# Optimization experiments

Measured on AMD Instinct MI355X. Metric: run time of the kernel, lower is better.

Reference implementation:

```python
import jax, jax.numpy as jnp
import numpy as np

N, V, H, LAT, OUT = 256, 256, 256, 64, 128
EPS = 1e-5

def setup_inputs() -> dict:
    key = jax.random.key(0)
    ks = jax.random.split(key, 16)
    s = lambda fan_in: 1.0 / np.sqrt(fan_in)
    gin = 2 * H + LAT  # GAT input size
    return {
        "obs": jax.random.normal(ks[0], (N, V, 5), jnp.float32),
        "high_intention": jax.random.normal(ks[1], (N, V, LAT), jnp.float32),
        "Ws": jax.random.uniform(ks[2], (2, H), jnp.float32, -s(2), s(2)),
        "bs": jax.random.uniform(ks[3], (H,), jnp.float32, -s(2), s(2)),
        "Wv": jax.random.uniform(ks[4], (2, H), jnp.float32, -s(2), s(2)),
        "bv": jax.random.uniform(ks[5], (H,), jnp.float32, -s(2), s(2)),
        "Wg": jax.random.uniform(ks[6], (gin, H), jnp.float32, -s(gin), s(gin)),
        "a_w": jax.random.uniform(ks[7], (2 * H,), jnp.float32, -s(2 * H), s(2 * H)),
        "W1": jax.random.uniform(ks[8], (2 * H, H), jnp.float32, -s(2 * H), s(2 * H)),
        "b1": jax.random.uniform(ks[9], (H,), jnp.float32, -s(2 * H), s(2 * H)),
        "g1": jnp.ones((H,), jnp.float32),
        "be1": jnp.zeros((H,), jnp.float32),
        "W2": jax.random.uniform(ks[10], (H, OUT), jnp.float32, -s(H), s(H)),
        "b2": jax.random.uniform(ks[11], (OUT,), jnp.float32, -s(H), s(H)),
        "g2": jnp.ones((OUT,), jnp.float32),
        "be2": jnp.zeros((OUT,), jnp.float32),
    }

def _batchnorm(x, g, b):
    # training-mode BatchNorm1d: batch stats, biased variance
    m = x.mean(0)
    v = x.var(0)
    return g * (x - m) / jnp.sqrt(v + EPS) + b

def reference(obs, high_intention, Ws, bs, Wv, bv, Wg, a_w, W1, b1, g1, be1, W2, b2, g2, be2):
    se = jax.nn.relu(obs[:, :, 1:3] @ Ws + bs)   # [N,V,H]
    ve = jax.nn.relu(obs[:, :, 3:5] @ Wv + bv)   # [N,V,H]
    comb = jnp.concatenate([se, ve, high_intention], axis=-1)  # [N,V,2H+LAT]
    h = comb @ Wg                                 # [N,V,H]
    hdim = Ws.shape[1]
    a1, a2 = a_w[:hdim], a_w[hdim:]
    # e_ij = leaky_relu(a . [h_i, h_j]) = leaky_relu(h_i.a1 + h_j.a2)
    e = jax.nn.leaky_relu((h @ a1)[:, :, None] + (h @ a2)[:, None, :], 0.01)  # [N,V,V]
    att = jax.nn.softmax(e, axis=2)
    h_prime = jnp.einsum('nij,njh->nih', att, h)  # [N,V,H]
    cf = jnp.concatenate([h_prime, se], axis=-1).reshape(-1, 2 * hdim)
    x = jax.nn.relu(_batchnorm(cf @ W1 + b1, g1, be1))
    x = jax.nn.relu(_batchnorm(x @ W2 + b2, g2, be2))
    return x.reshape(obs.shape[0], obs.shape[1], -1)
```

## Files before the change

### kernel.cpp

```cpp
#include <hip/hip_runtime.h>
#include <math.h>

namespace {

constexpr int kH = 256, kOut = 128;
constexpr int kNV = 65536;
constexpr float kEps = 1e-5f;

typedef __attribute__((ext_vector_type(8))) short bf16x8;
typedef __attribute__((ext_vector_type(4))) float f32x4;
typedef unsigned int u32;

__device__ inline short f2bf(float f) {
  union { float f; u32 u; } v; v.f = f;
  u32 r = v.u + 0x7fffu + ((v.u >> 16) & 1u);
  return (short)(r >> 16);
}
__device__ inline float bf2f(short s) {
  union { float f; u32 u; } v; v.u = ((u32)(unsigned short)s) << 16; return v.f;
}

__global__ __launch_bounds__(256) void kpack(
    const float* __restrict__ Wg, const float* __restrict__ W1,
    const float* __restrict__ W2, const float* __restrict__ a_w,
    short* __restrict__ wgp, short* __restrict__ w1p, short* __restrict__ w2p,
    short* __restrict__ wgab, float* __restrict__ st)
{
  const int bid = blockIdx.x, t = threadIdx.x;
  if (bid >= 152) {
    const int b = bid - 152;
    if (t < 144) {
      const int col = t & 1, k = b * 72 + (t >> 1);
      if (k < 576) {
        const float* rowp = Wg + (size_t)k * 256;
        const float* ap = a_w + col * 256;
        float s0 = 0.f, s1 = 0.f, s2 = 0.f, s3 = 0.f;
        for (int c = 0; c < 256; c += 4) {
          s0 = fmaf(rowp[c+0], ap[c+0], s0);
          s1 = fmaf(rowp[c+1], ap[c+1], s1);
          s2 = fmaf(rowp[c+2], ap[c+2], s2);
          s3 = fmaf(rowp[c+3], ap[c+3], s3);
        }
        const int ks = k >> 5, r = k & 31, hq = r >> 3, e = r & 7;
        wgab[((ks*2 + col)*4 + hq)*8 + e] = f2bf((s0 + s1) + (s2 + s3));
      }
    }
    return;
  }
  if (bid == 0) {
#pragma unroll
    for (int i = 0; i < 6; ++i) st[i*256 + t] = 0.f;
  }
  const int uid = bid * 256 + t;
  const float* src; short* dst; int N; int u;
  if (uid < 18432)            { src = Wg; dst = wgp; N = 256; u = uid; }
  else if (uid < 34816)       { src = W1; dst = w1p; N = 256; u = uid - 18432; }
  else if (uid < 38912)       { src = W2; dst = w2p; N = 128; u = uid - 34816; }
  else return;
  const int lane = u & 63, ctkt = u >> 6;
  const int nct = N >> 4;
  const int kt = ctkt / nct, ct = ctkt % nct;
  const int row = kt * 32 + (lane >> 4) * 8;
  const int col = ct * 16 + (lane & 15);
  bf16x8 ov;
#pragma unroll
  for (int e = 0; e < 8; ++e) ov[e] = f2bf(src[(size_t)(row + e) * N + col]);
  *reinterpret_cast<bf16x8*>(dst + (size_t)u * 8) = ov;
}

__global__ __launch_bounds__(256, 4) void k1_encode(
    const float* __restrict__ obs, const float* __restrict__ hin,
    const float* __restrict__ Ws, const float* __restrict__ bs,
    const float* __restrict__ Wv, const float* __restrict__ bv,
    const short* __restrict__ wgp, const short* __restrict__ wgab,
    short* __restrict__ hpack, float* __restrict__ ha1, float* __restrict__ ha2)
{
  __shared__ __align__(16) short comb[32][584];
  __shared__ float obs_s[32][4];
  const int t = threadIdx.x;
  const int xcd = blockIdx.x & 7, ib = blockIdx.x >> 3;
  const int workid = xcd * 256 + ib;
  const int r0 = workid * 32;

  if (t < 128) obs_s[t >> 2][t & 3] = obs[(size_t)(r0 + (t >> 2)) * 5 + 1 + (t & 3)];
#pragma unroll
  for (int jj = 0; jj < 2; ++jj) {
    const int f = jj * 1024 + t * 4;
    const int row = f >> 6, c = f & 63;
    const float4 v = *reinterpret_cast<const float4*>(hin + (size_t)r0 * 64 + f);
    short4 o;
    o.x = f2bf(v.x); o.y = f2bf(v.y); o.z = f2bf(v.z); o.w = f2bf(v.w);
    *reinterpret_cast<short4*>(&comb[row][512 + c]) = o;
  }
  const float ws0 = Ws[t], ws1 = Ws[256 + t], bsv = bs[t];
  const float wv0 = Wv[t], wv1 = Wv[256 + t], bvv = bv[t];
  __syncthreads();
  for (int r = 0; r < 32; ++r) {
    const float o1 = obs_s[r][0], o2 = obs_s[r][1], o3 = obs_s[r][2], o4 = obs_s[r][3];
    const float sv = fmaf(o2, ws1, fmaf(o1, ws0, bsv));
    comb[r][t] = f2bf(fmaxf(sv, 0.f));
    const float vv = fmaf(o4, wv1, fmaf(o3, wv0, bvv));
    comb[r][256 + t] = f2bf(fmaxf(vv, 0.f));
  }
  __syncthreads();

  const int w = t >> 6, lane = t & 63, lo = lane & 15, hq = lane >> 4;
  f32x4 acc[2][4];
  f32x4 accE[2];
#pragma unroll
  for (int rt = 0; rt < 2; ++rt) {
    accE[rt] = (f32x4){0.f, 0.f, 0.f, 0.f};
#pragma unroll
    for (int ct = 0; ct < 4; ++ct) acc[rt][ct] = (f32x4){0.f, 0.f, 0.f, 0.f};
  }

  const short* wB = wgp + ((size_t)(w*4)*64 + lane)*8;
  bf16x8 bb[4];
#pragma unroll
  for (int ct = 0; ct < 4; ++ct)
    bb[ct] = *reinterpret_cast<const bf16x8*>(wB + ct*512);

#pragma unroll
  for (int ks = 0; ks < 18; ++ks) {
    bf16x8 bn[4];
    if (ks < 17) {
#pragma unroll
      for (int ct = 0; ct < 4; ++ct)
        bn[ct] = *reinterpret_cast<const bf16x8*>(wB + (ks+1)*8192 + ct*512);
    }
    bf16x8 a[2];
#pragma unroll
    for (int rt = 0; rt < 2; ++rt)
      a[rt] = *reinterpret_cast<const bf16x8*>(&comb[rt*16 + lo][ks*32 + hq*8]);
#pragma unroll
    for (int rt = 0; rt < 2; ++rt)
#pragma unroll
      for (int ct = 0; ct < 4; ++ct)
        acc[rt][ct] = __builtin_amdgcn_mfma_f32_16x16x32_bf16(a[rt], bb[ct], acc[rt][ct], 0, 0, 0);
    if (w == 0) {
      bf16x8 be;
      if (lo < 2)
        be = *reinterpret_cast<const bf16x8*>(wgab + ((ks*2 + lo)*4 + hq)*8);
      else
        be = (bf16x8){0,0,0,0,0,0,0,0};
#pragma unroll
      for (int rt = 0; rt < 2; ++rt)
        accE[rt] = __builtin_amdgcn_mfma_f32_16x16x32_bf16(a[rt], be, accE[rt], 0, 0, 0);
    }
    if (ks < 17) {
#pragma unroll
      for (int ct = 0; ct < 4; ++ct) bb[ct] = bn[ct];
    }
  }
  if (w == 0 && lo < 2) {
    float* dst = (lo == 0) ? ha1 : ha2;
#pragma unroll
    for (int rt = 0; rt < 2; ++rt)
#pragma unroll
      for (int q = 0; q < 4; ++q)
        dst[r0 + rt*16 + hq*4 + q] = accE[rt][q];
  }
  __syncthreads();

  short* pimg = reinterpret_cast<short*>(&comb[0][0]);
#pragma unroll
  for (int rt = 0; rt < 2; ++rt)
#pragma unroll
    for (int ct = 0; ct < 4; ++ct) {
      const int base = (((w*4 + ct)*64) + (rt*2 + (hq>>1))*16 + lo)*8 + (hq&1)*4;
      short4 val;
      val.x = f2bf(acc[rt][ct][0]); val.y = f2bf(acc[rt][ct][1]);
      val.z = f2bf(acc[rt][ct][2]); val.w = f2bf(acc[rt][ct][3]);
      *reinterpret_cast<short4*>(pimg + base) = val;
    }
  __syncthreads();

  short* dst = hpack + (size_t)workid * 8192;
#pragma unroll
  for (int j = 0; j < 4; ++j)
    *reinterpret_cast<bf16x8*>(dst + j*2048 + t*8) =
        *reinterpret_cast<const bf16x8*>(pimg + j*2048 + t*8);
}

__global__ __launch_bounds__(256, 4) void k23_attn_fc1(
    const float* __restrict__ ha1g, const float* __restrict__ ha2g,
    const short* __restrict__ hpack, const float* __restrict__ obs,
    const float* __restrict__ Ws, const float* __restrict__ bs,
    const short* __restrict__ w1p, short* __restrict__ y, float* __restrict__ st)
{
  __shared__ __align__(16) short attimg[64][264];
  __shared__ float ws_s[768];
  __shared__ float ha2_s[256];
  __shared__ float ha1_s[64], rd_s[64];
  __shared__ float red[4][64];
  __shared__ float obs_s[64][2];
  const int t = threadIdx.x;
  const int xcd = blockIdx.x & 7, ib = blockIdx.x >> 3;
  const int workid = xcd * 128 + ib;
  const int r0 = workid * 64;
  const int n = r0 >> 8;

  ws_s[t] = Ws[t]; ws_s[256 + t] = Ws[256 + t]; ws_s[512 + t] = bs[t];
  ha2_s[t] = ha2g[n*256 + t];
  if (t < 64) ha1_s[t] = ha1g[r0 + t];
  if (t < 128) obs_s[t >> 1][t & 1] = obs[(size_t)(r0 + (t >> 1)) * 5 + 1 + (t & 1)];
  __syncthreads();

  const int rr = t & 63, seg = t >> 6;
  {
    const float a1 = ha1_s[rr];
    float sum = 0.f;
    for (int c8 = 0; c8 < 8; ++c8) {
      bf16x8 pk;
#pragma unroll
      for (int e = 0; e < 8; ++e) {
        float x = a1 + ha2_s[seg*64 + c8*8 + e];
        x = fmaxf(x, 0.01f * x);
        const float ev = __expf(x);
        sum += ev;
        pk[e] = f2bf(ev);
      }
      *reinterpret_cast<bf16x8*>(&attimg[rr][seg*64 + c8*8]) = pk;
    }
    red[seg][rr] = sum;
  }
  __syncthreads();
  if (t < 64) rd_s[t] = 1.f / (red[0][t] + red[1][t] + red[2][t] + red[3][t]);
  __syncthreads();

  const int w = t >> 6, lane = t & 63, lo = lane & 15, hq = lane >> 4;
  f32x4 acc[4][4];
#pragma unroll
  for (int rt = 0; rt < 4; ++rt)
#pragma unroll
    for (int ct = 0; ct < 4; ++ct) acc[rt][ct] = (f32x4){0.f, 0.f, 0.f, 0.f};

  {
    const short* bB = hpack + (size_t)n*65536 + ((size_t)(w*4)*64 + lane)*8;
    bf16x8 bb[4];
#pragma unroll
    for (int ct = 0; ct < 4; ++ct) bb[ct] = *reinterpret_cast<const bf16x8*>(bB + ct*512);
    for (int ks = 0; ks < 8; ++ks) {
      bf16x8 bn[4];
      if (ks < 7) {
#pragma unroll
        for (int ct = 0; ct < 4; ++ct)
          bn[ct] = *reinterpret_cast<const bf16x8*>(bB + (ks+1)*8192 + ct*512);
      }
      bf16x8 a[4];
#pragma unroll
      for (int rt = 0; rt < 4; ++rt)
        a[rt] = *reinterpret_cast<const bf16x8*>(&attimg[rt*16 + lo][ks*32 + hq*8]);
#pragma unroll
      for (int rt = 0; rt < 4; ++rt)
#pragma unroll
        for (int ct = 0; ct < 4; ++ct)
          acc[rt][ct] = __builtin_amdgcn_mfma_f32_16x16x32_bf16(a[rt], bb[ct], acc[rt][ct], 0, 0, 0);
      if (ks < 7) {
#pragma unroll
        for (int ct = 0; ct < 4; ++ct) bb[ct] = bn[ct];
      }
    }
  }
  __syncthreads();

#pragma unroll
  for (int rt = 0; rt < 4; ++rt)
#pragma unroll
    for (int q = 0; q < 4; ++q) {
      const int row = rt*16 + hq*4 + q;
      const float sc = rd_s[row];
#pragma unroll
      for (int ct = 0; ct < 4; ++ct)
        attimg[row][w*64 + ct*16 + lo] = f2bf(acc[rt][ct][q] * sc);
    }
  __syncthreads();

  f32x4 accY[4][4];
#pragma unroll
  for (int rt = 0; rt < 4; ++rt)
#pragma unroll
    for (int ct = 0; ct < 4; ++ct) accY[rt][ct] = (f32x4){0.f, 0.f, 0.f, 0.f};
  const short* w1B = w1p + ((size_t)(w*4)*64 + lane)*8;
  {
    bf16x8 bb[4];
#pragma unroll
    for (int ct = 0; ct < 4; ++ct) bb[ct] = *reinterpret_cast<const bf16x8*>(w1B + ct*512);
    for (int ks = 0; ks < 8; ++ks) {
      bf16x8 bn[4];
      if (ks < 7) {
#pragma unroll
        for (int ct = 0; ct < 4; ++ct)
          bn[ct] = *reinterpret_cast<const bf16x8*>(w1B + (ks+1)*8192 + ct*512);
      }
      bf16x8 a[4];
#pragma unroll
      for (int rt = 0; rt < 4; ++rt)
        a[rt] = *reinterpret_cast<const bf16x8*>(&attimg[rt*16 + lo][ks*32 + hq*8]);
#pragma unroll
      for (int rt = 0; rt < 4; ++rt)
#pragma unroll
        for (int ct = 0; ct < 4; ++ct)
          accY[rt][ct] = __builtin_amdgcn_mfma_f32_16x16x32_bf16(a[rt], bb[ct], accY[rt][ct], 0, 0, 0);
      if (ks < 7) {
#pragma unroll
        for (int ct = 0; ct < 4; ++ct) bb[ct] = bn[ct];
      }
    }
  }
  __syncthreads();

  {
    const float o1 = obs_s[rr][0], o2 = obs_s[rr][1];
    for (int c8 = 0; c8 < 8; ++c8) {
      const int c = seg*64 + c8*8;
      bf16x8 pk;
#pragma unroll
      for (int e = 0; e < 8; ++e) {
        const float sv = fmaf(o2, ws_s[256 + c + e], fmaf(o1, ws_s[c + e], ws_s[512 + c + e]));
        pk[e] = f2bf(fmaxf(sv, 0.f));
      }
      *reinterpret_cast<bf16x8*>(&attimg[rr][c]) = pk;
    }
  }
  __syncthreads();

  {
    bf16x8 bb[4];
#pragma unroll
    for (int ct = 0; ct < 4; ++ct)
      bb[ct] = *reinterpret_cast<const bf16x8*>(w1B + 8*8192 + ct*512);
    for (int ks = 0; ks < 8; ++ks) {
      bf16x8 bn[4];
      if (ks < 7) {
#pragma unroll
        for (int ct = 0; ct < 4; ++ct)
          bn[ct] = *reinterpret_cast<const bf16x8*>(w1B + (ks+9)*8192 + ct*512);
      }
      bf16x8 a[4];
#pragma unroll
      for (int rt = 0; rt < 4; ++rt)
        a[rt] = *reinterpret_cast<const bf16x8*>(&attimg[rt*16 + lo][ks*32 + hq*8]);
#pragma unroll
      for (int rt = 0; rt < 4; ++rt)
#pragma unroll
        for (int ct = 0; ct < 4; ++ct)
          accY[rt][ct] = __builtin_amdgcn_mfma_f32_16x16x32_bf16(a[rt], bb[ct], accY[rt][ct], 0, 0, 0);
      if (ks < 7) {
#pragma unroll
        for (int ct = 0; ct < 4; ++ct) bb[ct] = bn[ct];
      }
    }
  }

  float s[4] = {0,0,0,0}, ss[4] = {0,0,0,0};
#pragma unroll
  for (int rt = 0; rt < 4; ++rt)
#pragma unroll
    for (int q = 0; q < 4; ++q)
#pragma unroll
      for (int ct = 0; ct < 4; ++ct) {
        const float v = accY[rt][ct][q];
        s[ct] += v; ss[ct] += v * v;
      }
#pragma unroll
  for (int off = 16; off < 64; off <<= 1)
#pragma unroll
    for (int ct = 0; ct < 4; ++ct) {
      s[ct] += __shfl_xor(s[ct], off);
      ss[ct] += __shfl_xor(ss[ct], off);
    }
  if (hq == 0)
#pragma unroll
    for (int ct = 0; ct < 4; ++ct) {
      const int col = w*64 + ct*16 + lo;
      atomicAdd(&st[col], s[ct]);
      atomicAdd(&st[256 + col], ss[ct]);
    }
  __syncthreads();

#pragma unroll
  for (int rt = 0; rt < 4; ++rt)
#pragma unroll
    for (int q = 0; q < 4; ++q) {
      const int row = rt*16 + hq*4 + q;
#pragma unroll
      for (int ct = 0; ct < 4; ++ct)
        attimg[row][w*64 + ct*16 + lo] = f2bf(accY[rt][ct][q]);
    }
  __syncthreads();
  const short* img = &attimg[0][0];
#pragma unroll
  for (int j = 0; j < 8; ++j) {
    const int f = j*2048 + t*8, row = f >> 8, col = f & 255;
    *reinterpret_cast<bf16x8*>(y + (size_t)(r0 + row)*256 + col) =
        *reinterpret_cast<const bf16x8*>(img + row*264 + col);
  }
}

__global__ __launch_bounds__(256) void k5_z(
    const short* __restrict__ y, const short* __restrict__ w2p,
    const float* __restrict__ g1, const float* __restrict__ be1,
    float* __restrict__ st, short* __restrict__ zb)
{
  __shared__ __align__(16) short xs[64][264];
  __shared__ float sc_s[256], sh_s[256];
  const int t = threadIdx.x;
  const int r0 = blockIdx.x * 64;
  {
    const float mean = st[t] * (1.f / kNV);
    const float var  = st[256 + t] * (1.f / kNV) - mean * mean;
    const float sc   = g1[t] / sqrtf(var + kEps);
    sc_s[t] = sc; sh_s[t] = be1[t] - mean * sc;
  }
  __syncthreads();
#pragma unroll
  for (int j = 0; j < 8; ++j) {
    const int f = j*2048 + t*8, row = f >> 8, col = f & 255;
    bf16x8 v = *reinterpret_cast<const bf16x8*>(y + (size_t)(r0 + row)*256 + col);
    bf16x8 ov;
#pragma unroll
    for (int e = 0; e < 8; ++e) {
      const float fv = fmaf(bf2f(v[e]), sc_s[col + e], sh_s[col + e]);
      ov[e] = f2bf(fmaxf(fv, 0.f));
    }
    *reinterpret_cast<bf16x8*>(&xs[row][col]) = ov;
  }
  __syncthreads();

  const int w = t >> 6, lane = t & 63, lo = lane & 15, hq = lane >> 4;
  f32x4 acc[4][2];
#pragma unroll
  for (int rt = 0; rt < 4; ++rt)
#pragma unroll
    for (int ct = 0; ct < 2; ++ct) acc[rt][ct] = (f32x4){0.f, 0.f, 0.f, 0.f};

  {
    const short* w2B = w2p + ((size_t)(w*2)*64 + lane)*8;
    bf16x8 bb[2];
#pragma unroll
    for (int ct = 0; ct < 2; ++ct) bb[ct] = *reinterpret_cast<const bf16x8*>(w2B + ct*512);
    for (int ks = 0; ks < 8; ++ks) {
      bf16x8 bn[2];
      if (ks < 7) {
#pragma unroll
        for (int ct = 0; ct < 2; ++ct)
          bn[ct] = *reinterpret_cast<const bf16x8*>(w2B + (ks+1)*4096 + ct*512);
      }
      bf16x8 a[4];
#pragma unroll
      for (int rt = 0; rt < 4; ++rt)
        a[rt] = *reinterpret_cast<const bf16x8*>(&xs[rt*16 + lo][ks*32 + hq*8]);
#pragma unroll
      for (int rt = 0; rt < 4; ++rt)
#pragma unroll
        for (int ct = 0; ct < 2; ++ct)
          acc[rt][ct] = __builtin_amdgcn_mfma_f32_16x16x32_bf16(a[rt], bb[ct], acc[rt][ct], 0, 0, 0);
      if (ks < 7) {
#pragma unroll
        for (int ct = 0; ct < 2; ++ct) bb[ct] = bn[ct];
      }
    }
  }

  float s[2] = {0,0}, ss[2] = {0,0};
#pragma unroll
  for (int rt = 0; rt < 4; ++rt)
#pragma unroll
    for (int q = 0; q < 4; ++q)
#pragma unroll
      for (int ct = 0; ct < 2; ++ct) {
        const float v = acc[rt][ct][q];
        s[ct] += v; ss[ct] += v * v;
      }
#pragma unroll
  for (int off = 16; off < 64; off <<= 1)
#pragma unroll
    for (int ct = 0; ct < 2; ++ct) {
      s[ct] += __shfl_xor(s[ct], off);
      ss[ct] += __shfl_xor(ss[ct], off);
    }
  if (hq == 0)
#pragma unroll
    for (int ct = 0; ct < 2; ++ct) {
      const int col = w*32 + ct*16 + lo;
      atomicAdd(&st[1024 + col], s[ct]);
      atomicAdd(&st[1152 + col], ss[ct]);
    }
  __syncthreads();

  short* zimg = reinterpret_cast<short*>(&xs[0][0]);
#pragma unroll
  for (int rt = 0; rt < 4; ++rt)
#pragma unroll
    for (int q = 0; q < 4; ++q) {
      const int row = rt*16 + hq*4 + q;
#pragma unroll
      for (int ct = 0; ct < 2; ++ct)
        zimg[row*136 + w*32 + ct*16 + lo] = f2bf(acc[rt][ct][q]);
    }
  __syncthreads();
#pragma unroll
  for (int j = 0; j < 4; ++j) {
    const int f = j*2048 + t*8, row = f >> 7, col = f & 127;
    *reinterpret_cast<bf16x8*>(zb + (size_t)(r0 + row)*128 + col) =
        *reinterpret_cast<const bf16x8*>(zimg + row*136 + col);
  }
}

__global__ __launch_bounds__(256) void k7_out(
    const short* __restrict__ zb, const float* __restrict__ st,
    const float* __restrict__ g2, const float* __restrict__ be2,
    float* __restrict__ out)
{
  __shared__ float sc_s[128], sh_s[128];
  const int t = threadIdx.x;
  if (t < 128) {
    const float mean = st[1024 + t] * (1.f / kNV);
    const float var  = st[1152 + t] * (1.f / kNV) - mean * mean;
    const float sc   = g2[t] / sqrtf(var + kEps);
    sc_s[t] = sc; sh_s[t] = be2[t] - mean * sc;
  }
  __syncthreads();
#pragma unroll
  for (int j = 0; j < 2; ++j) {
    const size_t u = (size_t)blockIdx.x * 512 + j*256 + t;
    bf16x8 v = *reinterpret_cast<const bf16x8*>(zb + u*8);
    const int col = ((int)u & 15) * 8;
    float4 r0, r1;
    r0.x = fmaxf(fmaf(bf2f(v[0]), sc_s[col+0], sh_s[col+0]), 0.f);
    r0.y = fmaxf(fmaf(bf2f(v[1]), sc_s[col+1], sh_s[col+1]), 0.f);
    r0.z = fmaxf(fmaf(bf2f(v[2]), sc_s[col+2], sh_s[col+2]), 0.f);
    r0.w = fmaxf(fmaf(bf2f(v[3]), sc_s[col+3], sh_s[col+3]), 0.f);
    r1.x = fmaxf(fmaf(bf2f(v[4]), sc_s[col+4], sh_s[col+4]), 0.f);
    r1.y = fmaxf(fmaf(bf2f(v[5]), sc_s[col+5], sh_s[col+5]), 0.f);
    r1.z = fmaxf(fmaf(bf2f(v[6]), sc_s[col+6], sh_s[col+6]), 0.f);
    r1.w = fmaxf(fmaf(bf2f(v[7]), sc_s[col+7], sh_s[col+7]), 0.f);
    *reinterpret_cast<float4*>(out + u*8)     = r0;
    *reinterpret_cast<float4*>(out + u*8 + 4) = r1;
  }
}

}

extern "C" void kernel_launch(void* const* d_in, const int* in_sizes, int n_in,
                              void* d_out, int out_size, void* d_ws, size_t ws_size,
                              hipStream_t stream) {
  const float* obs = (const float*)d_in[0];
  const float* hin = (const float*)d_in[1];
  const float* Ws  = (const float*)d_in[2];
  const float* bs  = (const float*)d_in[3];
  const float* Wv  = (const float*)d_in[4];
  const float* bv  = (const float*)d_in[5];
  const float* Wg  = (const float*)d_in[6];
  const float* a_w = (const float*)d_in[7];
  const float* W1  = (const float*)d_in[8];
  const float* g1  = (const float*)d_in[10];
  const float* be1 = (const float*)d_in[11];
  const float* W2  = (const float*)d_in[12];
  const float* g2  = (const float*)d_in[14];
  const float* be2 = (const float*)d_in[15];

  char* base = (char*)d_ws;
  short* hpack = (short*)(base);
  short* y     = (short*)(base + 33554432);
  short* zb    = (short*)(base + 67108864);
  float* ha1   = (float*)(base + 83886080);
  float* ha2   = (float*)(base + 84148224);
  float* st    = (float*)(base + 84410368);
  short* wgp   = (short*)(base + 84416512);
  short* w1p   = (short*)(base + 84711424);
  short* w2p   = (short*)(base + 84973568);
  short* wgab  = (short*)(base + 85039104);
  float* out   = (float*)d_out;

  kpack       <<<160,  256, 0, stream>>>(Wg, W1, W2, a_w, wgp, w1p, w2p, wgab, st);
  k1_encode   <<<2048, 256, 0, stream>>>(obs, hin, Ws, bs, Wv, bv, wgp, wgab, hpack, ha1, ha2);
  k23_attn_fc1<<<1024, 256, 0, stream>>>(ha1, ha2, hpack, obs, Ws, bs, w1p, y, st);
  k5_z        <<<1024, 256, 0, stream>>>(y, w2p, g1, be1, st, zb);
  k7_out      <<<2048, 256, 0, stream>>>(zb, st, g2, be2, out);
}
```

Baseline: 138.7 us.

## Fuse attention, FC1, FC2 and output into one cooperative kernel with grid syncs

Replaces the three kernels for attention+FC1, BN1+FC2 and BN2+output with one cooperative kernel of 512 blocks. Each block handles 128 rows in two 64-row halves and keeps the FC1 and FC2 results packed as bf16 in registers, using grid.sync to wait for the global BatchNorm statistics. This removes the y and zb round trips through global memory and two kernel launches. In exchange it needs a large register footprint at 2 blocks per CU, relies on a cooperative launch succeeding (the old path remains as fallback), and adds grid-wide barrier cost.

After: 248.8 us. 79.3% more time.

```diff
diff --git a/kernel.cpp b/kernel.cpp
--- a/kernel.cpp
+++ b/kernel.cpp
@@ -1,5 +1,8 @@
 #include <hip/hip_runtime.h>
+#include <hip/hip_cooperative_groups.h>
 #include <math.h>
+
+namespace cg = cooperative_groups;
 
 namespace {
 
@@ -182,6 +185,366 @@
         *reinterpret_cast<const bf16x8*>(pimg + j*2048 + t*8);
 }
 
+__global__ __launch_bounds__(256, 2) void kfused2(
+    const float* __restrict__ ha1g, const float* __restrict__ ha2g,
+    const short* __restrict__ hpack, const float* __restrict__ obs,
+    const float* __restrict__ Ws, const float* __restrict__ bs,
+    const short* __restrict__ w1p, const short* __restrict__ w2p,
+    const float* __restrict__ g1, const float* __restrict__ be1,
+    const float* __restrict__ g2, const float* __restrict__ be2,
+    float* __restrict__ st, float* __restrict__ out)
+{
+  __shared__ __align__(16) short attimg[64][264];
+  __shared__ float ws_s[768];
+  __shared__ float ha2_s[256];
+  __shared__ float ha1_s[128];
+  __shared__ float rd_s[128];
+  __shared__ float red[4][64];
+  __shared__ float obs_s[128][2];
+  cg::grid_group grid = cg::this_grid();
+  const int t = threadIdx.x;
+  const int xcd = blockIdx.x & 7, ibk = blockIdx.x >> 3;
+  const int workid = xcd * 64 + ibk;
+  const int R0 = workid * 128;
+  const int n = R0 >> 8;
+
+  ws_s[t] = Ws[t]; ws_s[256 + t] = Ws[256 + t]; ws_s[512 + t] = bs[t];
+  ha2_s[t] = ha2g[n*256 + t];
+  if (t < 128) ha1_s[t] = ha1g[R0 + t];
+  obs_s[t >> 1][t & 1] = obs[(size_t)(R0 + (t >> 1)) * 5 + 1 + (t & 1)];
+  __syncthreads();
+
+  const int rr = t & 63, seg = t >> 6;
+  const int w = t >> 6, lane = t & 63, lo = lane & 15, hq = lane >> 4;
+
+  u32 yp[2][4][4][2];
+  u32 zp[2][4][2][2];
+
+#pragma unroll
+  for (int s = 0; s < 2; ++s) {
+    {
+      const float a1 = ha1_s[s*64 + rr];
+      float sum = 0.f;
+      for (int c8 = 0; c8 < 8; ++c8) {
+        bf16x8 pk;
+#pragma unroll
+        for (int e = 0; e < 8; ++e) {
+          float x = a1 + ha2_s[seg*64 + c8*8 + e];
+          x = fmaxf(x, 0.01f * x);
+          const float ev = __expf(x);
+          sum += ev; pk[e] = f2bf(ev);
+        }
+        *reinterpret_cast<bf16x8*>(&attimg[rr][seg*64 + c8*8]) = pk;
+      }
+      red[seg][rr] = sum;
+    }
+    __syncthreads();
+    if (t < 64) rd_s[s*64 + t] = 1.f / (red[0][t] + red[1][t] + red[2][t] + red[3][t]);
+    __syncthreads();
+
+    f32x4 acc[4][4];
+#pragma unroll
+    for (int rt = 0; rt < 4; ++rt)
+#pragma unroll
+      for (int ct = 0; ct < 4; ++ct) acc[rt][ct] = (f32x4){0.f, 0.f, 0.f, 0.f};
+    {
+      const short* bB = hpack + (size_t)n*65536 + ((size_t)(w*4)*64 + lane)*8;
+      bf16x8 bb[4];
+#pragma unroll
+      for (int ct = 0; ct < 4; ++ct) bb[ct] = *reinterpret_cast<const bf16x8*>(bB + ct*512);
+      for (int ks = 0; ks < 8; ++ks) {
+        bf16x8 bn[4];
+        if (ks < 7) {
+#pragma unroll
+          for (int ct = 0; ct < 4; ++ct)
+            bn[ct] = *reinterpret_cast<const bf16x8*>(bB + (ks+1)*8192 + ct*512);
+        }
+        bf16x8 a[4];
+#pragma unroll
+        for (int rt = 0; rt < 4; ++rt)
+          a[rt] = *reinterpret_cast<const bf16x8*>(&attimg[rt*16 + lo][ks*32 + hq*8]);
+#pragma unroll
+        for (int rt = 0; rt < 4; ++rt)
+#pragma unroll
+          for (int ct = 0; ct < 4; ++ct)
+            acc[rt][ct] = __builtin_amdgcn_mfma_f32_16x16x32_bf16(a[rt], bb[ct], acc[rt][ct], 0, 0, 0);
+        if (ks < 7) {
+#pragma unroll
+          for (int ct = 0; ct < 4; ++ct) bb[ct] = bn[ct];
+        }
+      }
+    }
+    __syncthreads();
+
+#pragma unroll
+    for (int rt = 0; rt < 4; ++rt)
+#pragma unroll
+      for (int q = 0; q < 4; ++q) {
+        const int row = rt*16 + hq*4 + q;
+        const float sc = rd_s[s*64 + row];
+#pragma unroll
+        for (int ct = 0; ct < 4; ++ct)
+          attimg[row][w*64 + ct*16 + lo] = f2bf(acc[rt][ct][q] * sc);
+      }
+    __syncthreads();
+
+    f32x4 accY[4][4];
+#pragma unroll
+    for (int rt = 0; rt < 4; ++rt)
+#pragma unroll
+      for (int ct = 0; ct < 4; ++ct) accY[rt][ct] = (f32x4){0.f, 0.f, 0.f, 0.f};
+    const short* w1B = w1p + ((size_t)(w*4)*64 + lane)*8;
+    {
+      bf16x8 bb[4];
+#pragma unroll
+      for (int ct = 0; ct < 4; ++ct) bb[ct] = *reinterpret_cast<const bf16x8*>(w1B + ct*512);
+      for (int ks = 0; ks < 8; ++ks) {
+        bf16x8 bn[4];
+        if (ks < 7) {
+#pragma unroll
+          for (int ct = 0; ct < 4; ++ct)
+            bn[ct] = *reinterpret_cast<const bf16x8*>(w1B + (ks+1)*8192 + ct*512);
+        }
+        bf16x8 a[4];
+#pragma unroll
+        for (int rt = 0; rt < 4; ++rt)
+          a[rt] = *reinterpret_cast<const bf16x8*>(&attimg[rt*16 + lo][ks*32 + hq*8]);
+#pragma unroll
+        for (int rt = 0; rt < 4; ++rt)
+#pragma unroll
+          for (int ct = 0; ct < 4; ++ct)
+            accY[rt][ct] = __builtin_amdgcn_mfma_f32_16x16x32_bf16(a[rt], bb[ct], accY[rt][ct], 0, 0, 0);
+        if (ks < 7) {
+#pragma unroll
+          for (int ct = 0; ct < 4; ++ct) bb[ct] = bn[ct];
+        }
+      }
+    }
+    __syncthreads();
+
+    {
+      const float o1 = obs_s[s*64 + rr][0], o2 = obs_s[s*64 + rr][1];
+      for (int c8 = 0; c8 < 8; ++c8) {
+        const int c = seg*64 + c8*8;
+        bf16x8 pk;
+#pragma unroll
+        for (int e = 0; e < 8; ++e) {
+          const float sv = fmaf(o2, ws_s[256 + c + e], fmaf(o1, ws_s[c + e], ws_s[512 + c + e]));
+          pk[e] = f2bf(fmaxf(sv, 0.f));
+        }
+        *reinterpret_cast<bf16x8*>(&attimg[rr][c]) = pk;
+      }
+    }
+    __syncthreads();
+
+    {
+      bf16x8 bb[4];
+#pragma unroll
+      for (int ct = 0; ct < 4; ++ct)
+        bb[ct] = *reinterpret_cast<const bf16x8*>(w1B + 8*8192 + ct*512);
+      for (int ks = 0; ks < 8; ++ks) {
+        bf16x8 bn[4];
+        if (ks < 7) {
+#pragma unroll
+          for (int ct = 0; ct < 4; ++ct)
+            bn[ct] = *reinterpret_cast<const bf16x8*>(w1B + (ks+9)*8192 + ct*512);
+        }
+        bf16x8 a[4];
+#pragma unroll
+        for (int rt = 0; rt < 4; ++rt)
+          a[rt] = *reinterpret_cast<const bf16x8*>(&attimg[rt*16 + lo][ks*32 + hq*8]);
+#pragma unroll
+        for (int rt = 0; rt < 4; ++rt)
+#pragma unroll
+          for (int ct = 0; ct < 4; ++ct)
+            accY[rt][ct] = __builtin_amdgcn_mfma_f32_16x16x32_bf16(a[rt], bb[ct], accY[rt][ct], 0, 0, 0);
+        if (ks < 7) {
+#pragma unroll
+          for (int ct = 0; ct < 4; ++ct) bb[ct] = bn[ct];
+        }
+      }
+    }
+
+    {
+      float sm[4] = {0,0,0,0}, ssm[4] = {0,0,0,0};
+#pragma unroll
+      for (int rt = 0; rt < 4; ++rt)
+#pragma unroll
+        for (int q = 0; q < 4; ++q)
+#pragma unroll
+          for (int ct = 0; ct < 4; ++ct) {
+            const float v = accY[rt][ct][q];
+            sm[ct] += v; ssm[ct] += v * v;
+          }
+#pragma unroll
+      for (int off = 16; off < 64; off <<= 1)
+#pragma unroll
+        for (int ct = 0; ct < 4; ++ct) {
+          sm[ct] += __shfl_xor(sm[ct], off);
+          ssm[ct] += __shfl_xor(ssm[ct], off);
+        }
+      if (hq == 0)
+#pragma unroll
+        for (int ct = 0; ct < 4; ++ct) {
+          const int col = w*64 + ct*16 + lo;
+          atomicAdd(&st[col], sm[ct]);
+          atomicAdd(&st[256 + col], ssm[ct]);
+        }
+    }
+
+#pragma unroll
+    for (int rt = 0; rt < 4; ++rt)
+#pragma unroll
+      for (int ct = 0; ct < 4; ++ct) {
+        yp[s][rt][ct][0] = (u32)(unsigned short)f2bf(accY[rt][ct][0]) |
+                           ((u32)(unsigned short)f2bf(accY[rt][ct][1]) << 16);
+        yp[s][rt][ct][1] = (u32)(unsigned short)f2bf(accY[rt][ct][2]) |
+                           ((u32)(unsigned short)f2bf(accY[rt][ct][3]) << 16);
+      }
+    __syncthreads();
+  }
+
+  grid.sync();
+
+  {
+    const float mean = st[t] * (1.f / kNV);
+    const float var  = st[256 + t] * (1.f / kNV) - mean * mean;
+    const float sc   = g1[t] / sqrtf(var + kEps);
+    ws_s[t] = sc; ws_s[256 + t] = be1[t] - mean * sc;
+  }
+  __syncthreads();
+
+#pragma unroll
+  for (int s = 0; s < 2; ++s) {
+    float sc_[4], sh_[4];
+#pragma unroll
+    for (int ct = 0; ct < 4; ++ct) {
+      const int col = w*64 + ct*16 + lo;
+      sc_[ct] = ws_s[col]; sh_[ct] = ws_s[256 + col];
+    }
+#pragma unroll
+    for (int rt = 0; rt < 4; ++rt)
+#pragma unroll
+      for (int ct = 0; ct < 4; ++ct) {
+        const u32 p0 = yp[s][rt][ct][0], p1 = yp[s][rt][ct][1];
+        const int row = rt*16 + hq*4;
+        const int col = w*64 + ct*16 + lo;
+        attimg[row+0][col] = f2bf(fmaxf(fmaf(bf2f((short)p0),        sc_[ct], sh_[ct]), 0.f));
+        attimg[row+1][col] = f2bf(fmaxf(fmaf(bf2f((short)(p0 >> 16)), sc_[ct], sh_[ct]), 0.f));
+        attimg[row+2][col] = f2bf(fmaxf(fmaf(bf2f((short)p1),        sc_[ct], sh_[ct]), 0.f));
+        attimg[row+3][col] = f2bf(fmaxf(fmaf(bf2f((short)(p1 >> 16)), sc_[ct], sh_[ct]), 0.f));
+      }
+    __syncthreads();
+
+    f32x4 accZ[4][2];
+#pragma unroll
+    for (int rt = 0; rt < 4; ++rt)
+#pragma unroll
+      for (int ct = 0; ct < 2; ++ct) accZ[rt][ct] = (f32x4){0.f, 0.f, 0.f, 0.f};
+    {
+      const short* w2B = w2p + ((size_t)(w*2)*64 + lane)*8;
+      bf16x8 bb[2];
+#pragma unroll
+      for (int ct = 0; ct < 2; ++ct) bb[ct] = *reinterpret_cast<const bf16x8*>(w2B + ct*512);
+      for (int ks = 0; ks < 8; ++ks) {
+        bf16x8 bn[2];
+        if (ks < 7) {
+#pragma unroll
+          for (int ct = 0; ct < 2; ++ct)
+            bn[ct] = *reinterpret_cast<const bf16x8*>(w2B + (ks+1)*4096 + ct*512);
+        }
+        bf16x8 a[4];
+#pragma unroll
+        for (int rt = 0; rt < 4; ++rt)
+          a[rt] = *reinterpret_cast<const bf16x8*>(&attimg[rt*16 + lo][ks*32 + hq*8]);
+#pragma unroll
+        for (int rt = 0; rt < 4; ++rt)
+#pragma unroll
+          for (int ct = 0; ct < 2; ++ct)
+            accZ[rt][ct] = __builtin_amdgcn_mfma_f32_16x16x32_bf16(a[rt], bb[ct], accZ[rt][ct], 0, 0, 0);
+        if (ks < 7) {
+#pragma unroll
+          for (int ct = 0; ct < 2; ++ct) bb[ct] = bn[ct];
+        }
+      }
+    }
+
+    {
+      float sm[2] = {0,0}, ssm[2] = {0,0};
+#pragma unroll
+      for (int rt = 0; rt < 4; ++rt)
+#pragma unroll
+        for (int q = 0; q < 4; ++q)
+#pragma unroll
+          for (int ct = 0; ct < 2; ++ct) {
+            const float v = accZ[rt][ct][q];
+            sm[ct] += v; ssm[ct] += v * v;
+          }
+#pragma unroll
+      for (int off = 16; off < 64; off <<= 1)
+#pragma unroll
+        for (int ct = 0; ct < 2; ++ct) {
+          sm[ct] += __shfl_xor(sm[ct], off);
+          ssm[ct] += __shfl_xor(ssm[ct], off);
+        }
+      if (hq == 0)
+#pragma unroll
+        for (int ct = 0; ct < 2; ++ct) {
+          const int col = w*32 + ct*16 + lo;
+          atomicAdd(&st[1024 + col], sm[ct]);
+          atomicAdd(&st[1152 + col], ssm[ct]);
+        }
+    }
+
+#pragma unroll
+    for (int rt = 0; rt < 4; ++rt)
+#pragma unroll
+      for (int ct = 0; ct < 2; ++ct) {
+        zp[s][rt][ct][0] = (u32)(unsigned short)f2bf(accZ[rt][ct][0]) |
+                           ((u32)(unsigned short)f2bf(accZ[rt][ct][1]) << 16);
+        zp[s][rt][ct][1] = (u32)(unsigned short)f2bf(accZ[rt][ct][2]) |
+                           ((u32)(unsigned short)f2bf(accZ[rt][ct][3]) << 16);
+      }
+    __syncthreads();
+  }
+
+  grid.sync();
+
+  if (t < 128) {
+    const float mean = st[1024 + t] * (1.f / kNV);
+    const float var  = st[1152 + t] * (1.f / kNV) - mean * mean;
+    const float sc   = g2[t] / sqrtf(var + kEps);
+    ws_s[t] = sc; ws_s[128 + t] = be2[t] - mean * sc;
+  }
+  __syncthreads();
+
+  float* zimg = reinterpret_cast<float*>(&attimg[0][0]);
+#pragma unroll
+  for (int s = 0; s < 2; ++s) {
+#pragma unroll
+    for (int rt = 0; rt < 4; ++rt)
+#pragma unroll
+      for (int ct = 0; ct < 2; ++ct) {
+        const int col = w*32 + ct*16 + lo;
+        const float sc = ws_s[col], sh = ws_s[128 + col];
+        const u32 p0 = zp[s][rt][ct][0], p1 = zp[s][rt][ct][1];
+        const int row = rt*16 + hq*4;
+        zimg[(row+0)*132 + col] = fmaxf(fmaf(bf2f((short)p0),        sc, sh), 0.f);
+        zimg[(row+1)*132 + col] = fmaxf(fmaf(bf2f((short)(p0 >> 16)), sc, sh), 0.f);
+        zimg[(row+2)*132 + col] = fmaxf(fmaf(bf2f((short)p1),        sc, sh), 0.f);
+        zimg[(row+3)*132 + col] = fmaxf(fmaf(bf2f((short)(p1 >> 16)), sc, sh), 0.f);
+      }
+    __syncthreads();
+#pragma unroll
+    for (int j = 0; j < 8; ++j) {
+      const int f = j*1024 + t*4, row = f >> 7, col = f & 127;
+      *reinterpret_cast<float4*>(out + (size_t)(R0 + s*64 + row)*128 + col) =
+          *reinterpret_cast<const float4*>(zimg + row*132 + col);
+    }
+    __syncthreads();
+  }
+}
+
 __global__ __launch_bounds__(256, 4) void k23_attn_fc1(
     const float* __restrict__ ha1g, const float* __restrict__ ha2g,
     const short* __restrict__ hpack, const float* __restrict__ obs,
@@ -353,7 +716,7 @@
     }
   }
 
-  float s[4] = {0,0,0,0}, ss[4] = {0,0,0,0};
+  float sm[4] = {0,0,0,0}, ssm[4] = {0,0,0,0};
 #pragma unroll
   for (int rt = 0; rt < 4; ++rt)
 #pragma unroll
@@ -361,21 +724,21 @@
 #pragma unroll
       for (int ct = 0; ct < 4; ++ct) {
         const float v = accY[rt][ct][q];
-        s[ct] += v; ss[ct] += v * v;
+        sm[ct] += v; ssm[ct] += v * v;
       }
 #pragma unroll
   for (int off = 16; off < 64; off <<= 1)
 #pragma unroll
     for (int ct = 0; ct < 4; ++ct) {
-      s[ct] += __shfl_xor(s[ct], off);
-      ss[ct] += __shfl_xor(ss[ct], off);
+      sm[ct] += __shfl_xor(sm[ct], off);
+      ssm[ct] += __shfl_xor(ssm[ct], off);
     }
   if (hq == 0)
 #pragma unroll
     for (int ct = 0; ct < 4; ++ct) {
       const int col = w*64 + ct*16 + lo;
-      atomicAdd(&st[col], s[ct]);
-      atomicAdd(&st[256 + col], ss[ct]);
+      atomicAdd(&st[col], sm[ct]);
+      atomicAdd(&st[256 + col], ssm[ct]);
     }
   __syncthreads();
 
@@ -463,7 +826,7 @@
     }
   }
 
-  float s[2] = {0,0}, ss[2] = {0,0};
+  float sm[2] = {0,0}, ssm[2] = {0,0};
 #pragma unroll
   for (int rt = 0; rt < 4; ++rt)
 #pragma unroll
@@ -471,21 +834,21 @@
 #pragma unroll
       for (int ct = 0; ct < 2; ++ct) {
         const float v = acc[rt][ct][q];
-        s[ct] += v; ss[ct] += v * v;
+        sm[ct] += v; ssm[ct] += v * v;
       }
 #pragma unroll
   for (int off = 16; off < 64; off <<= 1)
 #pragma unroll
     for (int ct = 0; ct < 2; ++ct) {
-      s[ct] += __shfl_xor(s[ct], off);
-      ss[ct] += __shfl_xor(ss[ct], off);
+      sm[ct] += __shfl_xor(sm[ct], off);
+      ssm[ct] += __shfl_xor(ssm[ct], off);
     }
   if (hq == 0)
 #pragma unroll
     for (int ct = 0; ct < 2; ++ct) {
       const int col = w*32 + ct*16 + lo;
-      atomicAdd(&st[1024 + col], s[ct]);
-      atomicAdd(&st[1152 + col], ss[ct]);
+      atomicAdd(&st[1024 + col], sm[ct]);
+      atomicAdd(&st[1152 + col], ssm[ct]);
     }
   __syncthreads();
 
@@ -574,9 +937,19 @@
   short* wgab  = (short*)(base + 85039104);
   float* out   = (float*)d_out;
 
-  kpack       <<<160,  256, 0, stream>>>(Wg, W1, W2, a_w, wgp, w1p, w2p, wgab, st);
-  k1_encode   <<<2048, 256, 0, stream>>>(obs, hin, Ws, bs, Wv, bv, wgp, wgab, hpack, ha1, ha2);
-  k23_attn_fc1<<<1024, 256, 0, stream>>>(ha1, ha2, hpack, obs, Ws, bs, w1p, y, st);
-  k5_z        <<<1024, 256, 0, stream>>>(y, w2p, g1, be1, st, zb);
-  k7_out      <<<2048, 256, 0, stream>>>(zb, st, g2, be2, out);
+  kpack    <<<160,  256, 0, stream>>>(Wg, W1, W2, a_w, wgp, w1p, w2p, wgab, st);
+  k1_encode<<<2048, 256, 0, stream>>>(obs, hin, Ws, bs, Wv, bv, wgp, wgab, hpack, ha1, ha2);
+
+  void* kargs[] = {
+    (void*)&ha1, (void*)&ha2, (void*)&hpack, (void*)&obs, (void*)&Ws, (void*)&bs,
+    (void*)&w1p, (void*)&w2p, (void*)&g1, (void*)&be1, (void*)&g2, (void*)&be2,
+    (void*)&st, (void*)&out
+  };
+  hipError_t err = hipLaunchCooperativeKernel((const void*)kfused2, dim3(512), dim3(256),
+                                              kargs, 0, stream);
+  if (err != hipSuccess) {
+    k23_attn_fc1<<<1024, 256, 0, stream>>>(ha1, ha2, hpack, obs, Ws, bs, w1p, y, st);
+    k5_z        <<<1024, 256, 0, stream>>>(y, w2p, g1, be1, st, zb);
+    k7_out      <<<2048, 256, 0, stream>>>(zb, st, g2, be2, out);
+  }
 }
```
